# Optimization experiments

Measured on AMD Instinct MI355X. Metric: run time of the kernel, lower is better.

Reference implementation:

```python
import jax, jax.numpy as jnp
import numpy as np

RANK = 10
SLOPE = 0.01  # nn.LeakyReLU default negative_slope


def _leaky(x):
    return jnp.where(x >= 0, x, SLOPE * x)


def _synth(x, aw, ab, weight, bias, ns, w_lat, lid):
    # fmm_modulate_linear with activation='demod'
    c_out, c_in = weight.shape
    styles = aw @ w_lat + ab                      # [(c_in+c_out)*RANK]
    L = styles[: c_out * RANK].reshape(c_out, RANK)
    R = styles[c_out * RANK :].reshape(RANK, c_in)
    mod = (L @ R) * (1.0 / np.sqrt(RANK))          # [c_out, c_in]
    W = weight * (mod + 1.0)
    W = W / (jnp.linalg.norm(W, axis=1, keepdims=True) + 1e-8)
    out = x @ W.T + bias                           # [N, c_out]
    out = _leaky(out)
    noise = jax.random.normal(jax.random.fold_in(jax.random.key(42), lid),
                              out.shape, dtype=out.dtype)
    return out + noise * ns


def setup_inputs() -> dict:
    key = jax.random.key(0)
    N, E, H, IN, OUT, WD = 50000, 800000, 256, 128, 256, 512
    ks = jax.random.split(key, 24)
    s = lambda fan: 1.0 / np.sqrt(fan)
    syn = lambda k0, k1, k2, k3, ci, co: {
        'aw': jax.random.normal(k0, ((ci + co) * RANK, WD)) * s(WD),
        'ab': jnp.zeros(((ci + co) * RANK,)),
        'weight': jax.random.normal(k1, (co, ci)) * s(ci),
        'bias': jax.random.uniform(k2, (co,), minval=-s(ci), maxval=s(ci)),
    }
    le = syn(ks[0], ks[1], ks[2], ks[3], H, H)
    f1 = syn(ks[4], ks[5], ks[6], ks[7], H, H)
    f2 = syn(ks[8], ks[9], ks[10], ks[11], H, OUT)
    return {
        'x': jax.random.normal(ks[12], (N, IN)),
        'edge_index': jax.random.randint(ks[13], (2, E), 0, N, dtype=jnp.int32),
        'w': jax.random.normal(ks[14], (WD,)),
        'node_weight': jax.random.normal(ks[15], (N, H)) * s(N),
        'edge_bias': jax.random.uniform(ks[16], (H,), minval=-s(N), maxval=s(N)),
        'le_aw': le['aw'], 'le_ab': le['ab'], 'le_weight': le['weight'], 'le_bias': le['bias'],
        'le_ns': jnp.zeros(()),
        'cat1_w': jax.random.normal(ks[17], (H, H)) * s(H), 'cat1_b': jnp.zeros((H,)),
        'cat2_w': jax.random.normal(ks[18], (H, H)) * s(H), 'cat2_b': jnp.zeros((H,)),
        'nm_w': jax.random.normal(ks[19], (H, IN)) * s(IN), 'nm_b': jnp.zeros((H,)),
        'f1_aw': f1['aw'], 'f1_ab': f1['ab'], 'f1_weight': f1['weight'], 'f1_bias': f1['bias'],
        'f1_ns': jnp.zeros(()),
        'f2_aw': f2['aw'], 'f2_ab': f2['ab'], 'f2_weight': f2['weight'], 'f2_bias': f2['bias'],
        'f2_ns': jnp.zeros(()),
    }


def reference(x, edge_index, w, node_weight, edge_bias,
              le_aw, le_ab, le_weight, le_bias, le_ns,
              cat1_w, cat1_b, cat2_w, cat2_b, nm_w, nm_b,
              f1_aw, f1_ab, f1_weight, f1_bias, f1_ns,
              f2_aw, f2_ab, f2_weight, f2_bias, f2_ns):
    N = node_weight.shape[0]
    src, dst = edge_index[0], edge_index[1]
    # SparseLinear: scatter-add source node embeddings at destinations
    agg = jax.ops.segment_sum(node_weight[src], dst, num_segments=N) + edge_bias
    out = _synth(agg, le_aw, le_ab, le_weight, le_bias, le_ns, w, 0)
    out = out + (out @ cat1_w.T + cat1_b)
    xn = x @ nm_w.T + nm_b                        # node_mlp (single linear)
    out = out + xn + (xn @ cat2_w.T + cat2_b)
    out = _leaky(out)
    out = _synth(out, f1_aw, f1_ab, f1_weight, f1_bias, f1_ns, w, 1)
    out = _synth(out, f2_aw, f2_ab, f2_weight, f2_bias, f2_ns, w, 2)
    return out
```

## Files before the change

kernel.cpp:

```cpp
#include <hip/hip_runtime.h>
#include <stdint.h>

#define HCH 256
#define INCH 128
#define WDIM 512
#define NRANK 10
#define SLOPE 0.01f

typedef __attribute__((ext_vector_type(16))) float f32x16;
typedef __attribute__((ext_vector_type(8))) short s16x8;

__device__ __forceinline__ float leaky(float v) { return v >= 0.f ? v : SLOPE * v; }

__device__ __forceinline__ void splitf(float v, ushort& h, ushort& l) {
  uint32_t u = __float_as_uint(v);
  uint32_t r = u + 0x7FFFu + ((u >> 16) & 1u);
  h = (ushort)(r >> 16);
  float hf = __uint_as_float((uint32_t)h << 16);
  float d = v - hf;
  uint32_t u2 = __float_as_uint(d);
  uint32_t r2 = u2 + 0x7FFFu + ((u2 >> 16) & 1u);
  l = (ushort)(r2 >> 16);
}

__device__ __forceinline__ int wsi(int o, int k) {
  return (k >> 5) * 8192 + ((k >> 4) & 1) * 4096 + ((k >> 3) & 1) * 2048 + o * 8 + (k & 7);
}

__global__ void k_styles(const float* __restrict__ aw0, const float* __restrict__ ab0,
                         const float* __restrict__ aw1, const float* __restrict__ ab1,
                         const float* __restrict__ aw2, const float* __restrict__ ab2,
                         const float* __restrict__ w, float* __restrict__ styles) {
  int wid = blockIdx.x * 4 + (threadIdx.x >> 6);
  int lane = threadIdx.x & 63;
  int s = wid / 5120;
  int r = wid - s * 5120;
  const float* aw = (s == 0) ? aw0 : (s == 1) ? aw1 : aw2;
  const float* ab = (s == 0) ? ab0 : (s == 1) ? ab1 : ab2;
  const float4* ap = (const float4*)(aw + (size_t)r * WDIM + lane * 8);
  const float4* wp = (const float4*)(w + lane * 8);
  float4 a0 = ap[0], a1 = ap[1], w0 = wp[0], w1 = wp[1];
  float sum = a0.x * w0.x + a0.y * w0.y + a0.z * w0.z + a0.w * w0.w +
              a1.x * w1.x + a1.y * w1.y + a1.z * w1.z + a1.w * w1.w;
#pragma unroll
  for (int off = 32; off > 0; off >>= 1) sum += __shfl_down(sum, off);
  if (lane == 0) styles[wid] = sum + ab[r];
}

__global__ void k_weights(const float* __restrict__ styles,
                          const float* __restrict__ wt0, const float* __restrict__ bs0,
                          const float* __restrict__ wt1, const float* __restrict__ bs1,
                          const float* __restrict__ wt2, const float* __restrict__ bs2,
                          ushort* __restrict__ Wh0, ushort* __restrict__ Wl0,
                          ushort* __restrict__ Wh1, ushort* __restrict__ Wl1,
                          ushort* __restrict__ Wh2, ushort* __restrict__ Wl2,
                          float* __restrict__ biasf) {
  int s = blockIdx.x >> 8;
  int o = blockIdx.x & 255;
  int k = threadIdx.x;
  const float* st = styles + s * 5120;
  const float* wt = (s == 0) ? wt0 : (s == 1) ? wt1 : wt2;
  const float* bs = (s == 0) ? bs0 : (s == 1) ? bs1 : bs2;
  ushort* Wh = (s == 0) ? Wh0 : (s == 1) ? Wh1 : Wh2;
  ushort* Wl = (s == 0) ? Wl0 : (s == 1) ? Wl1 : Wl2;
  float mod = 0.f;
#pragma unroll
  for (int r = 0; r < NRANK; r++)
    mod += st[o * NRANK + r] * st[HCH * NRANK + r * HCH + k];
  mod *= 0.31622776601683794f;
  float wv = wt[o * HCH + k] * (mod + 1.0f);
  __shared__ float red[HCH];
  red[k] = wv * wv;
  __syncthreads();
  for (int t = 128; t > 0; t >>= 1) {
    if (k < t) red[k] += red[k + t];
    __syncthreads();
  }
  float inv = 1.0f / (sqrtf(red[0]) + 1e-8f);
  ushort h, l;
  splitf(wv * inv, h, l);
  int idx = wsi(o, k);
  Wh[idx] = h;
  Wl[idx] = l;
  if (k == 0) biasf[s * HCH + o] = bs[o];
}

__global__ void k_prep(const float* __restrict__ cat1_w, const float* __restrict__ cat1_b,
                       const float* __restrict__ cat2_w, const float* __restrict__ cat2_b,
                       const float* __restrict__ nm_w, const float* __restrict__ nm_b,
                       ushort* __restrict__ M1h, ushort* __restrict__ M1l,
                       ushort* __restrict__ K2h, ushort* __restrict__ K2l,
                       float* __restrict__ b23) {
  int o = blockIdx.x;
  int t = threadIdx.x;
  for (int k = t; k < HCH; k += 128) {
    float m1v = cat1_w[o * HCH + k] + ((k == o) ? 1.f : 0.f);
    ushort h, l;
    splitf(m1v, h, l);
    int idx = wsi(o, k);
    M1h[idx] = h;
    M1l[idx] = l;
  }
  float acc = 0.f;
  for (int k = 0; k < HCH; k++) {
    float m2 = cat2_w[o * HCH + k] + ((k == o) ? 1.f : 0.f);
    acc += m2 * nm_w[k * INCH + t];
  }
  ushort h, l;
  splitf(acc, h, l);
  int idx = wsi(o, t);
  K2h[idx] = h;
  K2l[idx] = l;
  if (t == 0) {
    float bb = cat1_b[o] + cat2_b[o];
    for (int k = 0; k < HCH; k++)
      bb += (cat2_w[o * HCH + k] + ((k == o) ? 1.f : 0.f)) * nm_b[k];
    b23[o] = bb;
  }
}

__global__ void k_zero(int* __restrict__ p, int n) {
  int i = blockIdx.x * blockDim.x + threadIdx.x;
  if (i < n) p[i] = 0;
}
__global__ void k_hist(const int* __restrict__ ei, int* __restrict__ cnt, int E) {
  int e = blockIdx.x * blockDim.x + threadIdx.x;
  if (e < E) atomicAdd(&cnt[ei[E + e]], 1);
}
__global__ void k_bsum(const int* __restrict__ cnt, int* __restrict__ bsum, int N) {
  __shared__ int red[256];
  int t = threadIdx.x;
  int i = blockIdx.x * 256 + t;
  red[t] = (i < N) ? cnt[i] : 0;
  __syncthreads();
  for (int d = 128; d > 0; d >>= 1) {
    if (t < d) red[t] += red[t + d];
    __syncthreads();
  }
  if (t == 0) bsum[blockIdx.x] = red[0];
}
__global__ void k_scanb(int* __restrict__ bsum, int* __restrict__ offsets, int NB,
                        int N, int E) {
  __shared__ int s[256];
  int t = threadIdx.x;
  int v = (t < NB) ? bsum[t] : 0;
  s[t] = v;
  __syncthreads();
  for (int d = 1; d < 256; d <<= 1) {
    int tv = (t >= d) ? s[t - d] : 0;
    __syncthreads();
    s[t] += tv;
    __syncthreads();
  }
  if (t < NB) bsum[t] = s[t] - v;
  if (t == 0) offsets[N] = E;
}
__global__ void k_scanseg(int* __restrict__ cnt, const int* __restrict__ bsum,
                          int* __restrict__ offsets, int N) {
  __shared__ int s[256];
  int t = threadIdx.x;
  int i = blockIdx.x * 256 + t;
  int v = (i < N) ? cnt[i] : 0;
  s[t] = v;
  __syncthreads();
  for (int d = 1; d < 256; d <<= 1) {
    int tv = (t >= d) ? s[t - d] : 0;
    __syncthreads();
    s[t] += tv;
    __syncthreads();
  }
  if (i < N) {
    offsets[i] = bsum[blockIdx.x] + s[t] - v;
    cnt[i] = 0;
  }
}
__global__ void k_place(const int* __restrict__ ei, const int* __restrict__ offsets,
                        int* __restrict__ cur, int* __restrict__ csr, int E) {
  int e = blockIdx.x * blockDim.x + threadIdx.x;
  if (e >= E) return;
  int dst = ei[E + e];
  int pos = atomicAdd(&cur[dst], 1);
  csr[offsets[dst] + pos] = ei[e];
}

__global__ void k_pull(const int* __restrict__ csr, const int* __restrict__ offsets,
                       const float* __restrict__ nw, const float* __restrict__ eb,
                       float* __restrict__ agg, int Mc) {
  int wid = blockIdx.x * 4 + (threadIdx.x >> 6);
  if (wid >= Mc) return;
  int lane = threadIdx.x & 63;
  int s0 = offsets[wid], s1 = offsets[wid + 1];
  float4 a0 = *(const float4*)(eb + lane * 4);
  float4 a1 = make_float4(0.f, 0.f, 0.f, 0.f);
  float4 a2 = make_float4(0.f, 0.f, 0.f, 0.f);
  float4 a3 = make_float4(0.f, 0.f, 0.f, 0.f);
  int j = s0;
  for (; j + 3 < s1; j += 4) {
    int sa = csr[j], sb = csr[j + 1], sc = csr[j + 2], sd = csr[j + 3];
    float4 va = *(const float4*)(nw + (size_t)sa * HCH + lane * 4);
    float4 vb = *(const float4*)(nw + (size_t)sb * HCH + lane * 4);
    float4 vc = *(const float4*)(nw + (size_t)sc * HCH + lane * 4);
    float4 vd = *(const float4*)(nw + (size_t)sd * HCH + lane * 4);
    a0.x += va.x; a0.y += va.y; a0.z += va.z; a0.w += va.w;
    a1.x += vb.x; a1.y += vb.y; a1.z += vb.z; a1.w += vb.w;
    a2.x += vc.x; a2.y += vc.y; a2.z += vc.z; a2.w += vc.w;
    a3.x += vd.x; a3.y += vd.y; a3.z += vd.z; a3.w += vd.w;
  }
  for (; j < s1; j++) {
    int sa = csr[j];
    float4 va = *(const float4*)(nw + (size_t)sa * HCH + lane * 4);
    a0.x += va.x; a0.y += va.y; a0.z += va.z; a0.w += va.w;
  }
  a0.x += a1.x + a2.x + a3.x;
  a0.y += a1.y + a2.y + a3.y;
  a0.z += a1.z + a2.z + a3.z;
  a0.w += a1.w + a2.w + a3.w;
  *(float4*)(agg + (size_t)wid * HCH + lane * 4) = a0;
}


#define CHUNK(PH, PL, c)                                                        \
  {                                                                             \
    const char* _bh = (const char*)(PH) + (c) * 16384 + wlane;                  \
    const char* _bl = (const char*)(PL) + (c) * 16384 + wlane;                  \
    s16x8 bh0 = *(const s16x8*)(_bh);                                           \
    s16x8 bl0 = *(const s16x8*)(_bl);                                           \
    s16x8 bh1 = *(const s16x8*)(_bh + 8192);                                    \
    s16x8 bl1 = *(const s16x8*)(_bl + 8192);                                    \
    int _s0 = (((c) * 4 + kh) ^ cl) << 4;                                       \
    int _s1 = (((c) * 4 + 2 + kh) ^ cl) << 4;                                   \
    s16x8 a0h = *(const s16x8*)(actH + aoff0 + _s0);                            \
    s16x8 a0l = *(const s16x8*)(actL + aoff0 + _s0);                            \
    s16x8 a1h = *(const s16x8*)(actH + aoff1 + _s0);                            \
    s16x8 a1l = *(const s16x8*)(actL + aoff1 + _s0);                            \
    acc0 = __builtin_amdgcn_mfma_f32_32x32x16_bf16(a0h, bh0, acc0, 0, 0, 0);    \
    acc0 = __builtin_amdgcn_mfma_f32_32x32x16_bf16(a0h, bl0, acc0, 0, 0, 0);    \
    acc0 = __builtin_amdgcn_mfma_f32_32x32x16_bf16(a0l, bh0, acc0, 0, 0, 0);    \
    acc1 = __builtin_amdgcn_mfma_f32_32x32x16_bf16(a1h, bh0, acc1, 0, 0, 0);    \
    acc1 = __builtin_amdgcn_mfma_f32_32x32x16_bf16(a1h, bl0, acc1, 0, 0, 0);    \
    acc1 = __builtin_amdgcn_mfma_f32_32x32x16_bf16(a1l, bh0, acc1, 0, 0, 0);    \
    s16x8 c0h = *(const s16x8*)(actH + aoff0 + _s1);                            \
    s16x8 c0l = *(const s16x8*)(actL + aoff0 + _s1);                            \
    s16x8 c1h = *(const s16x8*)(actH + aoff1 + _s1);                            \
    s16x8 c1l = *(const s16x8*)(actL + aoff1 + _s1);                            \
    acc0 = __builtin_amdgcn_mfma_f32_32x32x16_bf16(c0h, bh1, acc0, 0, 0, 0);    \
    acc0 = __builtin_amdgcn_mfma_f32_32x32x16_bf16(c0h, bl1, acc0, 0, 0, 0);    \
    acc0 = __builtin_amdgcn_mfma_f32_32x32x16_bf16(c0l, bh1, acc0, 0, 0, 0);    \
    acc1 = __builtin_amdgcn_mfma_f32_32x32x16_bf16(c1h, bh1, acc1, 0, 0, 0);    \
    acc1 = __builtin_amdgcn_mfma_f32_32x32x16_bf16(c1h, bl1, acc1, 0, 0, 0);    \
    acc1 = __builtin_amdgcn_mfma_f32_32x32x16_bf16(c1l, bh1, acc1, 0, 0, 0);    \
  }

#define EPI_ACT(BIAS)                                                           \
  {                                                                             \
    int _col = w * 32 + cl;                                                     \
    float _bb = (BIAS)[_col];                                                   \
    int _cb = _col & ~1;                                                        \
    _Pragma("unroll") for (int r = 0; r < 16; r++) {                            \
      int _rowf = (r & 3) + 8 * (r >> 2) + 4 * kh;                              \
      _Pragma("unroll") for (int part = 0; part < 2; part++) {                  \
        int _row = part * 32 + _rowf;                                           \
        float _v = (part ? acc1[r] : acc0[r]) + _bb;                            \
        _v = _v >= 0.f ? _v : SLOPE * _v;                                       \
        ushort _h, _l;                                                          \
        splitf(_v, _h, _l);                                                     \
        uint32_t _hl = ((uint32_t)_h << 16) | (uint32_t)_l;                     \
        uint32_t _pr = __shfl_xor(_hl, 1);                                      \
        int _off = _row * 512 + (((_cb >> 3) ^ (_row & 31)) << 4) + (_cb & 7) * 2; \
        uint32_t _wd = (cl & 1) ? ((_pr & 0xFFFFu) | (_hl << 16))               \
                                : ((_hl >> 16) | (_pr & 0xFFFF0000u));          \
        char* _pl = (cl & 1) ? actL : actH;                                     \
        *(uint32_t*)(_pl + _off) = _wd;                                         \
      }                                                                         \
      acc0[r] = 0.f;                                                            \
      acc1[r] = 0.f;                                                            \
    }                                                                           \
  }

__global__ __launch_bounds__(512, 4) void k_fused(
    const float* __restrict__ agg, const float* __restrict__ x,
    const ushort* __restrict__ Wleh, const ushort* __restrict__ Wlel,
    const ushort* __restrict__ M1h, const ushort* __restrict__ M1l,
    const ushort* __restrict__ K2h, const ushort* __restrict__ K2l,
    const ushort* __restrict__ Wf1h, const ushort* __restrict__ Wf1l,
    const ushort* __restrict__ Wf2h, const ushort* __restrict__ Wf2l,
    const float* __restrict__ biasf, const float* __restrict__ b23,
    float* __restrict__ out, int Nn) {
  __shared__ __align__(16) char smem[65536];
  char* actH = smem;
  char* actL = smem + 32768;

  int tid = threadIdx.x;
  int lane = tid & 63;
  int w = tid >> 6;
  int cl = lane & 31;
  int kh = lane >> 5;
  int r0 = blockIdx.x * 64;

  const int wlane = kh * 4096 + (w * 32 + cl) * 16;
  const int aoff0 = cl * 512;
  const int aoff1 = (32 + cl) * 512;

  {
    int gr = tid >> 3;
    int gn = r0 + gr;
    if (gn >= Nn) gn = Nn - 1;
    int cb = 4 * (tid & 7);
    const float* ap = agg + (size_t)gn * HCH + cb;
#pragma unroll
    for (int q = 0; q < 8; q++) {
      float4 v = *(const float4*)(ap + 32 * q);
      int col = cb + 32 * q;
      ushort h0, l0, h1, l1, h2, l2, h3, l3;
      splitf(v.x, h0, l0); splitf(v.y, h1, l1);
      splitf(v.z, h2, l2); splitf(v.w, h3, l3);
      uint2 hh = make_uint2((uint32_t)h0 | ((uint32_t)h1 << 16),
                            (uint32_t)h2 | ((uint32_t)h3 << 16));
      uint2 ll = make_uint2((uint32_t)l0 | ((uint32_t)l1 << 16),
                            (uint32_t)l2 | ((uint32_t)l3 << 16));
      int off = gr * 512 + (((col >> 3) ^ (gr & 31)) << 4) + (col & 7) * 2;
      *(uint2*)(actH + off) = hh;
      *(uint2*)(actL + off) = ll;
    }
  }
  __syncthreads();

  f32x16 acc0, acc1;
#pragma unroll
  for (int i = 0; i < 16; i++) { acc0[i] = 0.f; acc1[i] = 0.f; }

#pragma unroll
  for (int c = 0; c < 8; c++) CHUNK(Wleh, Wlel, c);
  __syncthreads();
  EPI_ACT(biasf);
  __syncthreads();

#pragma unroll
  for (int c = 0; c < 8; c++) CHUNK(M1h, M1l, c);
  __syncthreads();
  {
    int gr = tid >> 3;
    int gn = r0 + gr;
    if (gn >= Nn) gn = Nn - 1;
    int cb = 4 * (tid & 7);
    const float* xp = x + (size_t)gn * INCH + cb;
#pragma unroll
    for (int q = 0; q < 4; q++) {
      float4 v = *(const float4*)(xp + 32 * q);
      int col = cb + 32 * q;
      ushort h0, l0, h1, l1, h2, l2, h3, l3;
      splitf(v.x, h0, l0); splitf(v.y, h1, l1);
      splitf(v.z, h2, l2); splitf(v.w, h3, l3);
      uint2 hh = make_uint2((uint32_t)h0 | ((uint32_t)h1 << 16),
                            (uint32_t)h2 | ((uint32_t)h3 << 16));
      uint2 ll = make_uint2((uint32_t)l0 | ((uint32_t)l1 << 16),
                            (uint32_t)l2 | ((uint32_t)l3 << 16));
      int off = gr * 512 + (((col >> 3) ^ (gr & 31)) << 4) + (col & 7) * 2;
      *(uint2*)(actH + off) = hh;
      *(uint2*)(actL + off) = ll;
    }
  }
  __syncthreads();

#pragma unroll
  for (int c = 0; c < 4; c++) CHUNK(K2h, K2l, c);
  __syncthreads();
  EPI_ACT(b23);
  __syncthreads();

#pragma unroll
  for (int c = 0; c < 8; c++) CHUNK(Wf1h, Wf1l, c);
  __syncthreads();
  EPI_ACT(biasf + HCH);
  __syncthreads();

#pragma unroll
  for (int c = 0; c < 8; c++) CHUNK(Wf2h, Wf2l, c);
  {
    const float* _bs = biasf + 2 * HCH;
    int col = w * 32 + cl;
    float bb = _bs[col];
#pragma unroll
    for (int r = 0; r < 16; r++) {
      int rowf = (r & 3) + 8 * (r >> 2) + 4 * kh;
      int g0 = r0 + rowf;
      int g1 = r0 + 32 + rowf;
      if (g0 < Nn) {
        float v = acc0[r] + bb;
        out[(size_t)g0 * HCH + col] = v >= 0.f ? v : SLOPE * v;
      }
      if (g1 < Nn) {
        float v = acc1[r] + bb;
        out[(size_t)g1 * HCH + col] = v >= 0.f ? v : SLOPE * v;
      }
    }
  }
}

extern "C" void kernel_launch(void* const* d_in, const int* in_sizes, int n_in,
                              void* d_out, int out_size, void* d_ws, size_t ws_size,
                              hipStream_t stream) {
  const float* x      = (const float*)d_in[0];
  const int*   ei     = (const int*)d_in[1];
  const float* w      = (const float*)d_in[2];
  const float* nw     = (const float*)d_in[3];
  const float* eb     = (const float*)d_in[4];
  const float* le_aw  = (const float*)d_in[5];
  const float* le_ab  = (const float*)d_in[6];
  const float* le_w   = (const float*)d_in[7];
  const float* le_b   = (const float*)d_in[8];
  const float* cat1_w = (const float*)d_in[10];
  const float* cat1_b = (const float*)d_in[11];
  const float* cat2_w = (const float*)d_in[12];
  const float* cat2_b = (const float*)d_in[13];
  const float* nm_w   = (const float*)d_in[14];
  const float* nm_b   = (const float*)d_in[15];
  const float* f1_aw  = (const float*)d_in[16];
  const float* f1_ab  = (const float*)d_in[17];
  const float* f1_w   = (const float*)d_in[18];
  const float* f1_b   = (const float*)d_in[19];
  const float* f2_aw  = (const float*)d_in[21];
  const float* f2_ab  = (const float*)d_in[22];
  const float* f2_w   = (const float*)d_in[23];
  const float* f2_b   = (const float*)d_in[24];

  const int N = in_sizes[3] / HCH;
  const int E = in_sizes[1] / 2;
  const int NB = (N + 255) / 256;

  uint8_t* ws = (uint8_t*)d_ws;
  float*  styles = (float*)(ws + 1024);
  float*  biasf  = (float*)(ws + 65536);
  float*  b23    = (float*)(ws + 69632);
  ushort* Wleh   = (ushort*)(ws + 131072);
  ushort* Wlel   = (ushort*)(ws + 262144);
  ushort* Wf1h   = (ushort*)(ws + 393216);
  ushort* Wf1l   = (ushort*)(ws + 524288);
  ushort* Wf2h   = (ushort*)(ws + 655360);
  ushort* Wf2l   = (ushort*)(ws + 786432);
  ushort* M1h    = (ushort*)(ws + 917504);
  ushort* M1l    = (ushort*)(ws + 1048576);
  ushort* K2h    = (ushort*)(ws + 1179648);
  ushort* K2l    = (ushort*)(ws + 1245184);
  int*    cnt    = (int*)(ws + 1376256);
  int*    bsum   = (int*)(ws + 1376256 + 262144);
  int*    offsets= (int*)(ws + 1376256 + 262144 + 4096);
  int*    csr    = (int*)(ws + 1376256 + 262144 + 4096 + 262144);
  size_t aggoff  = 1376256 + 262144 + 4096 + 262144 + (size_t)E * 4 + 65536;
  aggoff = (aggoff + 1023) & ~(size_t)1023;
  float*  agg    = (float*)(ws + aggoff);

  k_styles<<<3840, 256, 0, stream>>>(le_aw, le_ab, f1_aw, f1_ab, f2_aw, f2_ab, w, styles);
  k_weights<<<768, 256, 0, stream>>>(styles, le_w, le_b, f1_w, f1_b, f2_w, f2_b,
                                     Wleh, Wlel, Wf1h, Wf1l, Wf2h, Wf2l, biasf);
  k_prep<<<256, 128, 0, stream>>>(cat1_w, cat1_b, cat2_w, cat2_b, nm_w, nm_b,
                                  M1h, M1l, K2h, K2l, b23);

  int eb256 = (E + 255) / 256;
  k_zero<<<NB, 256, 0, stream>>>(cnt, N);
  k_hist<<<eb256, 256, 0, stream>>>(ei, cnt, E);
  k_bsum<<<NB, 256, 0, stream>>>(cnt, bsum, N);
  k_scanb<<<1, 256, 0, stream>>>(bsum, offsets, NB, N, E);
  k_scanseg<<<NB, 256, 0, stream>>>(cnt, bsum, offsets, N);
  k_place<<<eb256, 256, 0, stream>>>(ei, offsets, cnt, csr, E);

  k_pull<<<(N + 3) / 4, 256, 0, stream>>>(csr, offsets, nw, eb, agg, N);
  k_fused<<<(N + 63) / 64, 512, 0, stream>>>(agg, x,
                                             Wleh, Wlel, M1h, M1l, K2h, K2l,
                                             Wf1h, Wf1l, Wf2h, Wf2l,
                                             biasf, b23, (float*)d_out, N);
}
```

Baseline: 522.8 us.

## Merge setup kernels into persistent megakernel with grid barriers; prefetch weights in fused GEMM

Replaces the nine small preprocessing launches (styles, weight demodulation, cat/node-MLP prep, CSR histogram, scan and placement) with one persistent 256-block kernel whose phases are separated by a software grid barrier on an atomic counter. The aim is to remove per-launch overhead and idle gaps between the tiny kernels. Separately, the fused MFMA kernel now double-buffers the B-weight register loads one chunk ahead, including across stage boundaries, and raises wave priority around the MFMA groups to hide global load latency. Risks: the grid barrier deadlocks if all 256 blocks of 1024 threads cannot be co-resident. The extra prefetch registers may also lower occupancy of the fused kernel.

```diff
diff --git a/kernel.cpp b/kernel.cpp
--- a/kernel.cpp
+++ b/kernel.cpp
@@ -27,160 +27,213 @@
   return (k >> 5) * 8192 + ((k >> 4) & 1) * 4096 + ((k >> 3) & 1) * 2048 + o * 8 + (k & 7);
 }
 
-__global__ void k_styles(const float* __restrict__ aw0, const float* __restrict__ ab0,
-                         const float* __restrict__ aw1, const float* __restrict__ ab1,
-                         const float* __restrict__ aw2, const float* __restrict__ ab2,
-                         const float* __restrict__ w, float* __restrict__ styles) {
-  int wid = blockIdx.x * 4 + (threadIdx.x >> 6);
-  int lane = threadIdx.x & 63;
-  int s = wid / 5120;
-  int r = wid - s * 5120;
-  const float* aw = (s == 0) ? aw0 : (s == 1) ? aw1 : aw2;
-  const float* ab = (s == 0) ? ab0 : (s == 1) ? ab1 : ab2;
-  const float4* ap = (const float4*)(aw + (size_t)r * WDIM + lane * 8);
-  const float4* wp = (const float4*)(w + lane * 8);
-  float4 a0 = ap[0], a1 = ap[1], w0 = wp[0], w1 = wp[1];
-  float sum = a0.x * w0.x + a0.y * w0.y + a0.z * w0.z + a0.w * w0.w +
-              a1.x * w1.x + a1.y * w1.y + a1.z * w1.z + a1.w * w1.w;
-#pragma unroll
-  for (int off = 32; off > 0; off >>= 1) sum += __shfl_down(sum, off);
-  if (lane == 0) styles[wid] = sum + ab[r];
-}
-
-__global__ void k_weights(const float* __restrict__ styles,
-                          const float* __restrict__ wt0, const float* __restrict__ bs0,
-                          const float* __restrict__ wt1, const float* __restrict__ bs1,
-                          const float* __restrict__ wt2, const float* __restrict__ bs2,
-                          ushort* __restrict__ Wh0, ushort* __restrict__ Wl0,
-                          ushort* __restrict__ Wh1, ushort* __restrict__ Wl1,
-                          ushort* __restrict__ Wh2, ushort* __restrict__ Wl2,
-                          float* __restrict__ biasf) {
-  int s = blockIdx.x >> 8;
-  int o = blockIdx.x & 255;
-  int k = threadIdx.x;
-  const float* st = styles + s * 5120;
-  const float* wt = (s == 0) ? wt0 : (s == 1) ? wt1 : wt2;
-  const float* bs = (s == 0) ? bs0 : (s == 1) ? bs1 : bs2;
-  ushort* Wh = (s == 0) ? Wh0 : (s == 1) ? Wh1 : Wh2;
-  ushort* Wl = (s == 0) ? Wl0 : (s == 1) ? Wl1 : Wl2;
-  float mod = 0.f;
-#pragma unroll
-  for (int r = 0; r < NRANK; r++)
-    mod += st[o * NRANK + r] * st[HCH * NRANK + r * HCH + k];
-  mod *= 0.31622776601683794f;
-  float wv = wt[o * HCH + k] * (mod + 1.0f);
-  __shared__ float red[HCH];
-  red[k] = wv * wv;
-  __syncthreads();
-  for (int t = 128; t > 0; t >>= 1) {
-    if (k < t) red[k] += red[k + t];
-    __syncthreads();
-  }
-  float inv = 1.0f / (sqrtf(red[0]) + 1e-8f);
-  ushort h, l;
-  splitf(wv * inv, h, l);
-  int idx = wsi(o, k);
-  Wh[idx] = h;
-  Wl[idx] = l;
-  if (k == 0) biasf[s * HCH + o] = bs[o];
-}
-
-__global__ void k_prep(const float* __restrict__ cat1_w, const float* __restrict__ cat1_b,
-                       const float* __restrict__ cat2_w, const float* __restrict__ cat2_b,
-                       const float* __restrict__ nm_w, const float* __restrict__ nm_b,
-                       ushort* __restrict__ M1h, ushort* __restrict__ M1l,
-                       ushort* __restrict__ K2h, ushort* __restrict__ K2l,
-                       float* __restrict__ b23) {
-  int o = blockIdx.x;
-  int t = threadIdx.x;
-  for (int k = t; k < HCH; k += 128) {
-    float m1v = cat1_w[o * HCH + k] + ((k == o) ? 1.f : 0.f);
-    ushort h, l;
-    splitf(m1v, h, l);
-    int idx = wsi(o, k);
-    M1h[idx] = h;
-    M1l[idx] = l;
-  }
-  float acc = 0.f;
-  for (int k = 0; k < HCH; k++) {
-    float m2 = cat2_w[o * HCH + k] + ((k == o) ? 1.f : 0.f);
-    acc += m2 * nm_w[k * INCH + t];
-  }
-  ushort h, l;
-  splitf(acc, h, l);
-  int idx = wsi(o, t);
-  K2h[idx] = h;
-  K2l[idx] = l;
-  if (t == 0) {
-    float bb = cat1_b[o] + cat2_b[o];
-    for (int k = 0; k < HCH; k++)
+__device__ __forceinline__ void gbar(int* bar, int nblk) {
+  __syncthreads();
+  if (threadIdx.x == 0) {
+    int g = __hip_atomic_load(bar + 1, __ATOMIC_RELAXED, __HIP_MEMORY_SCOPE_AGENT);
+    __threadfence();
+    int a = __hip_atomic_fetch_add(bar, 1, __ATOMIC_ACQ_REL, __HIP_MEMORY_SCOPE_AGENT);
+    if (a == nblk - 1) {
+      __hip_atomic_store(bar, 0, __ATOMIC_RELAXED, __HIP_MEMORY_SCOPE_AGENT);
+      __hip_atomic_fetch_add(bar + 1, 1, __ATOMIC_RELEASE, __HIP_MEMORY_SCOPE_AGENT);
+    } else {
+      while (__hip_atomic_load(bar + 1, __ATOMIC_ACQUIRE, __HIP_MEMORY_SCOPE_AGENT) == g)
+        __builtin_amdgcn_s_sleep(8);
+    }
+  }
+  __syncthreads();
+  __threadfence();
+}
+
+__global__ __launch_bounds__(1024, 4) void k_mega(
+    const float* __restrict__ aw0, const float* __restrict__ ab0,
+    const float* __restrict__ aw1, const float* __restrict__ ab1,
+    const float* __restrict__ aw2, const float* __restrict__ ab2,
+    const float* __restrict__ wvec, float* __restrict__ styles,
+    const float* __restrict__ wt0, const float* __restrict__ bs0,
+    const float* __restrict__ wt1, const float* __restrict__ bs1,
+    const float* __restrict__ wt2, const float* __restrict__ bs2,
+    ushort* __restrict__ Wh0, ushort* __restrict__ Wl0,
+    ushort* __restrict__ Wh1, ushort* __restrict__ Wl1,
+    ushort* __restrict__ Wh2, ushort* __restrict__ Wl2,
+    float* __restrict__ biasf,
+    const float* __restrict__ cat1_w, const float* __restrict__ cat1_b,
+    const float* __restrict__ cat2_w, const float* __restrict__ cat2_b,
+    const float* __restrict__ nm_w, const float* __restrict__ nm_b,
+    ushort* __restrict__ M1h, ushort* __restrict__ M1l,
+    ushort* __restrict__ K2h, ushort* __restrict__ K2l,
+    float* __restrict__ b23,
+    const int* __restrict__ ei, int* __restrict__ cnt, int* __restrict__ bsum,
+    int* __restrict__ offsets, int* __restrict__ csr,
+    int* bar, int N, int E) {
+  int tid = threadIdx.x;
+  int lane = tid & 63;
+  int gw = blockIdx.x * 16 + (tid >> 6);
+  int gt = blockIdx.x * 1024 + tid;
+
+  for (int r = gw; r < 15360; r += 4096) {
+    int s = r / 5120;
+    int rr = r - s * 5120;
+    const float* aw = (s == 0) ? aw0 : (s == 1) ? aw1 : aw2;
+    const float* ab = (s == 0) ? ab0 : (s == 1) ? ab1 : ab2;
+    const float4* ap = (const float4*)(aw + (size_t)rr * WDIM + lane * 8);
+    const float4* wp = (const float4*)(wvec + lane * 8);
+    float4 a0 = ap[0], a1 = ap[1], w0 = wp[0], w1 = wp[1];
+    float sum = a0.x * w0.x + a0.y * w0.y + a0.z * w0.z + a0.w * w0.w +
+                a1.x * w1.x + a1.y * w1.y + a1.z * w1.z + a1.w * w1.w;
+#pragma unroll
+    for (int off = 32; off > 0; off >>= 1) sum += __shfl_down(sum, off);
+    if (lane == 0) styles[r] = sum + ab[rr];
+  }
+  if (gt < N) cnt[gt] = 0;
+  if (gt == 0) offsets[N] = E;
+  gbar(bar, 256);
+
+  if (gw < 768) {
+    int s = gw >> 8, o = gw & 255;
+    const float* st = styles + s * 5120;
+    const float* wt = (s == 0) ? wt0 : (s == 1) ? wt1 : wt2;
+    const float* bs = (s == 0) ? bs0 : (s == 1) ? bs1 : bs2;
+    ushort* Wh = (s == 0) ? Wh0 : (s == 1) ? Wh1 : Wh2;
+    ushort* Wl = (s == 0) ? Wl0 : (s == 1) ? Wl1 : Wl2;
+    int k0 = lane * 4;
+    float modv[4] = {0.f, 0.f, 0.f, 0.f};
+#pragma unroll
+    for (int r = 0; r < NRANK; r++) {
+      float a = st[o * NRANK + r];
+#pragma unroll
+      for (int j = 0; j < 4; j++) modv[j] += a * st[HCH * NRANK + r * HCH + k0 + j];
+    }
+    float wv[4];
+    float ssq = 0.f;
+#pragma unroll
+    for (int j = 0; j < 4; j++) {
+      wv[j] = wt[o * HCH + k0 + j] * (modv[j] * 0.31622776601683794f + 1.0f);
+      ssq += wv[j] * wv[j];
+    }
+#pragma unroll
+    for (int off = 32; off > 0; off >>= 1) ssq += __shfl_down(ssq, off);
+    ssq = __shfl(ssq, 0);
+    float inv = 1.0f / (sqrtf(ssq) + 1e-8f);
+#pragma unroll
+    for (int j = 0; j < 4; j++) {
+      ushort h, l;
+      splitf(wv[j] * inv, h, l);
+      int idx = wsi(o, k0 + j);
+      Wh[idx] = h;
+      Wl[idx] = l;
+    }
+    if (lane == 0) biasf[s * HCH + o] = bs[o];
+  } else if (gw < 1024) {
+    int o = gw - 768;
+    int k0 = lane * 4;
+#pragma unroll
+    for (int j = 0; j < 4; j++) {
+      int k = k0 + j;
+      float m1v = cat1_w[o * HCH + k] + ((k == o) ? 1.f : 0.f);
+      ushort h, l;
+      splitf(m1v, h, l);
+      int idx = wsi(o, k);
+      M1h[idx] = h;
+      M1l[idx] = l;
+    }
+    for (int tt = lane; tt < INCH; tt += 64) {
+      float acc = 0.f;
+      for (int k = 0; k < HCH; k++) {
+        float m2 = cat2_w[o * HCH + k] + ((k == o) ? 1.f : 0.f);
+        acc += m2 * nm_w[k * INCH + tt];
+      }
+      ushort h, l;
+      splitf(acc, h, l);
+      int idx = wsi(o, tt);
+      K2h[idx] = h;
+      K2l[idx] = l;
+    }
+    float bb = 0.f;
+    for (int k = lane; k < HCH; k += 64)
       bb += (cat2_w[o * HCH + k] + ((k == o) ? 1.f : 0.f)) * nm_b[k];
-    b23[o] = bb;
-  }
-}
-
-__global__ void k_zero(int* __restrict__ p, int n) {
-  int i = blockIdx.x * blockDim.x + threadIdx.x;
-  if (i < n) p[i] = 0;
-}
-__global__ void k_hist(const int* __restrict__ ei, int* __restrict__ cnt, int E) {
-  int e = blockIdx.x * blockDim.x + threadIdx.x;
-  if (e < E) atomicAdd(&cnt[ei[E + e]], 1);
-}
-__global__ void k_bsum(const int* __restrict__ cnt, int* __restrict__ bsum, int N) {
-  __shared__ int red[256];
-  int t = threadIdx.x;
-  int i = blockIdx.x * 256 + t;
-  red[t] = (i < N) ? cnt[i] : 0;
-  __syncthreads();
-  for (int d = 128; d > 0; d >>= 1) {
-    if (t < d) red[t] += red[t + d];
-    __syncthreads();
-  }
-  if (t == 0) bsum[blockIdx.x] = red[0];
-}
-__global__ void k_scanb(int* __restrict__ bsum, int* __restrict__ offsets, int NB,
-                        int N, int E) {
-  __shared__ int s[256];
-  int t = threadIdx.x;
-  int v = (t < NB) ? bsum[t] : 0;
-  s[t] = v;
-  __syncthreads();
-  for (int d = 1; d < 256; d <<= 1) {
-    int tv = (t >= d) ? s[t - d] : 0;
-    __syncthreads();
-    s[t] += tv;
-    __syncthreads();
-  }
-  if (t < NB) bsum[t] = s[t] - v;
-  if (t == 0) offsets[N] = E;
-}
-__global__ void k_scanseg(int* __restrict__ cnt, const int* __restrict__ bsum,
-                          int* __restrict__ offsets, int N) {
-  __shared__ int s[256];
-  int t = threadIdx.x;
-  int i = blockIdx.x * 256 + t;
-  int v = (i < N) ? cnt[i] : 0;
-  s[t] = v;
-  __syncthreads();
-  for (int d = 1; d < 256; d <<= 1) {
-    int tv = (t >= d) ? s[t - d] : 0;
-    __syncthreads();
-    s[t] += tv;
-    __syncthreads();
-  }
-  if (i < N) {
-    offsets[i] = bsum[blockIdx.x] + s[t] - v;
-    cnt[i] = 0;
-  }
-}
-__global__ void k_place(const int* __restrict__ ei, const int* __restrict__ offsets,
-                        int* __restrict__ cur, int* __restrict__ csr, int E) {
-  int e = blockIdx.x * blockDim.x + threadIdx.x;
-  if (e >= E) return;
-  int dst = ei[E + e];
-  int pos = atomicAdd(&cur[dst], 1);
-  csr[offsets[dst] + pos] = ei[e];
+#pragma unroll
+    for (int off = 32; off > 0; off >>= 1) bb += __shfl_down(bb, off);
+    if (lane == 0) b23[o] = cat1_b[o] + cat2_b[o] + bb;
+  } else {
+    int base = (gw - 1024) * 64 + lane;
+    for (int e = base; e < E; e += 3072 * 64) atomicAdd(&cnt[ei[E + e]], 1);
+  }
+  gbar(bar, 256);
+
+  int NCH = (N + 255) >> 8;
+  if (gw < NCH) {
+    int v = 0;
+#pragma unroll
+    for (int j = 0; j < 4; j++) {
+      int i = gw * 256 + lane + j * 64;
+      v += (i < N) ? cnt[i] : 0;
+    }
+#pragma unroll
+    for (int off = 32; off > 0; off >>= 1) v += __shfl_down(v, off);
+    if (lane == 0) bsum[gw] = v;
+  }
+  gbar(bar, 256);
+
+  if (gw == 0) {
+    int v[4];
+    int lsum = 0;
+#pragma unroll
+    for (int j = 0; j < 4; j++) {
+      int i = lane * 4 + j;
+      v[j] = (i < NCH) ? bsum[i] : 0;
+      lsum += v[j];
+    }
+    int inc = lsum;
+#pragma unroll
+    for (int d = 1; d < 64; d <<= 1) {
+      int t = __shfl_up(inc, d);
+      if (lane >= d) inc += t;
+    }
+    int run = inc - lsum;
+#pragma unroll
+    for (int j = 0; j < 4; j++) {
+      int i = lane * 4 + j;
+      int nv = v[j];
+      if (i < NCH) bsum[i] = run;
+      run += nv;
+    }
+  }
+  gbar(bar, 256);
+
+  if (gw < NCH) {
+    int v[4];
+    int lsum = 0;
+#pragma unroll
+    for (int j = 0; j < 4; j++) {
+      int i = gw * 256 + lane * 4 + j;
+      v[j] = (i < N) ? cnt[i] : 0;
+      lsum += v[j];
+    }
+    int inc = lsum;
+#pragma unroll
+    for (int d = 1; d < 64; d <<= 1) {
+      int t = __shfl_up(inc, d);
+      if (lane >= d) inc += t;
+    }
+    int run = bsum[gw] + inc - lsum;
+#pragma unroll
+    for (int j = 0; j < 4; j++) {
+      int i = gw * 256 + lane * 4 + j;
+      if (i < N) {
+        offsets[i] = run;
+        cnt[i] = 0;
+      }
+      run += v[j];
+    }
+  }
+  gbar(bar, 256);
+
+  for (int e = gt; e < E; e += 262144) {
+    int dst = ei[E + e];
+    int pos = atomicAdd(&cnt[dst], 1);
+    csr[offsets[dst] + pos] = ei[e];
+  }
 }
 
 __global__ void k_pull(const int* __restrict__ csr, const int* __restrict__ offsets,
@@ -219,36 +272,55 @@
 }
 
 
-#define CHUNK(PH, PL, c)                                                        \
+#define BLOADS(SH0, SL0, SH1, SL1, PH, PL, C)                                  \
+  {                                                                            \
+    const char* _bh = (const char*)(PH) + (C) * 16384 + wlane;                 \
+    const char* _bl = (const char*)(PL) + (C) * 16384 + wlane;                 \
+    SH0 = *(const s16x8*)(_bh);                                                \
+    SL0 = *(const s16x8*)(_bl);                                                \
+    SH1 = *(const s16x8*)(_bh + 8192);                                         \
+    SL1 = *(const s16x8*)(_bl + 8192);                                         \
+  }
+
+#define CMFMA(BH0, BL0, BH1, BL1, C)                                            \
   {                                                                             \
-    const char* _bh = (const char*)(PH) + (c) * 16384 + wlane;                  \
-    const char* _bl = (const char*)(PL) + (c) * 16384 + wlane;                  \
-    s16x8 bh0 = *(const s16x8*)(_bh);                                           \
-    s16x8 bl0 = *(const s16x8*)(_bl);                                           \
-    s16x8 bh1 = *(const s16x8*)(_bh + 8192);                                    \
-    s16x8 bl1 = *(const s16x8*)(_bl + 8192);                                    \
-    int _s0 = (((c) * 4 + kh) ^ cl) << 4;                                       \
-    int _s1 = (((c) * 4 + 2 + kh) ^ cl) << 4;                                   \
+    int _s0 = ((((C) * 4 + kh) ^ cl) << 4);                                     \
+    int _s1 = ((((C) * 4 + 2 + kh) ^ cl) << 4);                                 \
     s16x8 a0h = *(const s16x8*)(actH + aoff0 + _s0);                            \
     s16x8 a0l = *(const s16x8*)(actL + aoff0 + _s0);                            \
     s16x8 a1h = *(const s16x8*)(actH + aoff1 + _s0);                            \
     s16x8 a1l = *(const s16x8*)(actL + aoff1 + _s0);                            \
-    acc0 = __builtin_amdgcn_mfma_f32_32x32x16_bf16(a0h, bh0, acc0, 0, 0, 0);    \
-    acc0 = __builtin_amdgcn_mfma_f32_32x32x16_bf16(a0h, bl0, acc0, 0, 0, 0);    \
-    acc0 = __builtin_amdgcn_mfma_f32_32x32x16_bf16(a0l, bh0, acc0, 0, 0, 0);    \
-    acc1 = __builtin_amdgcn_mfma_f32_32x32x16_bf16(a1h, bh0, acc1, 0, 0, 0);    \
-    acc1 = __builtin_amdgcn_mfma_f32_32x32x16_bf16(a1h, bl0, acc1, 0, 0, 0);    \
-    acc1 = __builtin_amdgcn_mfma_f32_32x32x16_bf16(a1l, bh0, acc1, 0, 0, 0);    \
+    acc0 = __builtin_amdgcn_mfma_f32_32x32x16_bf16(a0h, BH0, acc0, 0, 0, 0);    \
+    acc0 = __builtin_amdgcn_mfma_f32_32x32x16_bf16(a0h, BL0, acc0, 0, 0, 0);    \
+    acc0 = __builtin_amdgcn_mfma_f32_32x32x16_bf16(a0l, BH0, acc0, 0, 0, 0);    \
+    acc1 = __builtin_amdgcn_mfma_f32_32x32x16_bf16(a1h, BH0, acc1, 0, 0, 0);    \
+    acc1 = __builtin_amdgcn_mfma_f32_32x32x16_bf16(a1h, BL0, acc1, 0, 0, 0);    \
+    acc1 = __builtin_amdgcn_mfma_f32_32x32x16_bf16(a1l, BH0, acc1, 0, 0, 0);    \
     s16x8 c0h = *(const s16x8*)(actH + aoff0 + _s1);                            \
     s16x8 c0l = *(const s16x8*)(actL + aoff0 + _s1);                            \
     s16x8 c1h = *(const s16x8*)(actH + aoff1 + _s1);                            \
     s16x8 c1l = *(const s16x8*)(actL + aoff1 + _s1);                            \
-    acc0 = __builtin_amdgcn_mfma_f32_32x32x16_bf16(c0h, bh1, acc0, 0, 0, 0);    \
-    acc0 = __builtin_amdgcn_mfma_f32_32x32x16_bf16(c0h, bl1, acc0, 0, 0, 0);    \
-    acc0 = __builtin_amdgcn_mfma_f32_32x32x16_bf16(c0l, bh1, acc0, 0, 0, 0);    \
-    acc1 = __builtin_amdgcn_mfma_f32_32x32x16_bf16(c1h, bh1, acc1, 0, 0, 0);    \
-    acc1 = __builtin_amdgcn_mfma_f32_32x32x16_bf16(c1h, bl1, acc1, 0, 0, 0);    \
-    acc1 = __builtin_amdgcn_mfma_f32_32x32x16_bf16(c1l, bh1, acc1, 0, 0, 0);    \
+    acc0 = __builtin_amdgcn_mfma_f32_32x32x16_bf16(c0h, BH1, acc0, 0, 0, 0);    \
+    acc0 = __builtin_amdgcn_mfma_f32_32x32x16_bf16(c0h, BL1, acc0, 0, 0, 0);    \
+    acc0 = __builtin_amdgcn_mfma_f32_32x32x16_bf16(c0l, BH1, acc0, 0, 0, 0);    \
+    acc1 = __builtin_amdgcn_mfma_f32_32x32x16_bf16(c1h, BH1, acc1, 0, 0, 0);    \
+    acc1 = __builtin_amdgcn_mfma_f32_32x32x16_bf16(c1h, BL1, acc1, 0, 0, 0);    \
+    acc1 = __builtin_amdgcn_mfma_f32_32x32x16_bf16(c1l, BH1, acc1, 0, 0, 0);    \
+  }
+
+#define STAGE(NC, PH, PL, NPH, NPL)                                             \
+  _Pragma("unroll")                                                             \
+  for (int c = 0; c < (NC); c += 2) {                                           \
+    __builtin_amdgcn_s_setprio(1);                                              \
+    CMFMA(pbh0, pbl0, pbh1, pbl1, c);                                           \
+    __builtin_amdgcn_s_setprio(0);                                              \
+    if (c + 2 < (NC)) { BLOADS(pbh0, pbl0, pbh1, pbl1, PH, PL, c + 2); }        \
+    else if ((NPH) != nullptr) { BLOADS(pbh0, pbl0, pbh1, pbl1, NPH, NPL, c + 2 - (NC)); } \
+    __builtin_amdgcn_s_setprio(1);                                              \
+    CMFMA(qbh0, qbl0, qbh1, qbl1, c + 1);                                       \
+    __builtin_amdgcn_s_setprio(0);                                              \
+    if (c + 3 < (NC)) { BLOADS(qbh0, qbl0, qbh1, qbl1, PH, PL, c + 3); }        \
+    else if ((NPH) != nullptr) { BLOADS(qbh0, qbl0, qbh1, qbl1, NPH, NPL, c + 3 - (NC)); } \
   }
 
 #define EPI_ACT(BIAS)                                                           \
@@ -301,6 +373,12 @@
   const int aoff0 = cl * 512;
   const int aoff1 = (32 + cl) * 512;
 
+  s16x8 pbh0, pbl0, pbh1, pbl1;
+  s16x8 qbh0, qbl0, qbh1, qbl1;
+
+  BLOADS(pbh0, pbl0, pbh1, pbl1, Wleh, Wlel, 0);
+  BLOADS(qbh0, qbl0, qbh1, qbl1, Wleh, Wlel, 1);
+
   {
     int gr = tid >> 3;
     int gn = r0 + gr;
@@ -329,14 +407,12 @@
 #pragma unroll
   for (int i = 0; i < 16; i++) { acc0[i] = 0.f; acc1[i] = 0.f; }
 
-#pragma unroll
-  for (int c = 0; c < 8; c++) CHUNK(Wleh, Wlel, c);
+  STAGE(8, Wleh, Wlel, M1h, M1l)
   __syncthreads();
   EPI_ACT(biasf);
   __syncthreads();
 
-#pragma unroll
-  for (int c = 0; c < 8; c++) CHUNK(M1h, M1l, c);
+  STAGE(8, M1h, M1l, K2h, K2l)
   __syncthreads();
   {
     int gr = tid >> 3;
@@ -362,20 +438,17 @@
   }
   __syncthreads();
 
-#pragma unroll
-  for (int c = 0; c < 4; c++) CHUNK(K2h, K2l, c);
+  STAGE(4, K2h, K2l, Wf1h, Wf1l)
   __syncthreads();
   EPI_ACT(b23);
   __syncthreads();
 
-#pragma unroll
-  for (int c = 0; c < 8; c++) CHUNK(Wf1h, Wf1l, c);
+  STAGE(8, Wf1h, Wf1l, Wf2h, Wf2l)
   __syncthreads();
   EPI_ACT(biasf + HCH);
   __syncthreads();
 
-#pragma unroll
-  for (int c = 0; c < 8; c++) CHUNK(Wf2h, Wf2l, c);
+  STAGE(8, Wf2h, Wf2l, (const ushort*)nullptr, (const ushort*)nullptr)
   {
     const float* _bs = biasf + 2 * HCH;
     int col = w * 32 + cl;
@@ -426,9 +499,9 @@
 
   const int N = in_sizes[3] / HCH;
   const int E = in_sizes[1] / 2;
-  const int NB = (N + 255) / 256;
 
   uint8_t* ws = (uint8_t*)d_ws;
+  int*    bar    = (int*)ws;
   float*  styles = (float*)(ws + 1024);
   float*  biasf  = (float*)(ws + 65536);
   float*  b23    = (float*)(ws + 69632);
@@ -450,20 +523,13 @@
   aggoff = (aggoff + 1023) & ~(size_t)1023;
   float*  agg    = (float*)(ws + aggoff);
 
-  k_styles<<<3840, 256, 0, stream>>>(le_aw, le_ab, f1_aw, f1_ab, f2_aw, f2_ab, w, styles);
-  k_weights<<<768, 256, 0, stream>>>(styles, le_w, le_b, f1_w, f1_b, f2_w, f2_b,
-                                     Wleh, Wlel, Wf1h, Wf1l, Wf2h, Wf2l, biasf);
-  k_prep<<<256, 128, 0, stream>>>(cat1_w, cat1_b, cat2_w, cat2_b, nm_w, nm_b,
-                                  M1h, M1l, K2h, K2l, b23);
-
-  int eb256 = (E + 255) / 256;
-  k_zero<<<NB, 256, 0, stream>>>(cnt, N);
-  k_hist<<<eb256, 256, 0, stream>>>(ei, cnt, E);
-  k_bsum<<<NB, 256, 0, stream>>>(cnt, bsum, N);
-  k_scanb<<<1, 256, 0, stream>>>(bsum, offsets, NB, N, E);
-  k_scanseg<<<NB, 256, 0, stream>>>(cnt, bsum, offsets, N);
-  k_place<<<eb256, 256, 0, stream>>>(ei, offsets, cnt, csr, E);
-
+  hipMemsetAsync(bar, 0, 64, stream);
+  k_mega<<<256, 1024, 0, stream>>>(le_aw, le_ab, f1_aw, f1_ab, f2_aw, f2_ab, w,
+                                   styles, le_w, le_b, f1_w, f1_b, f2_w, f2_b,
+                                   Wleh, Wlel, Wf1h, Wf1l, Wf2h, Wf2l, biasf,
+                                   cat1_w, cat1_b, cat2_w, cat2_b, nm_w, nm_b,
+                                   M1h, M1l, K2h, K2l, b23,
+                                   ei, cnt, bsum, offsets, csr, bar, N, E);
   k_pull<<<(N + 3) / 4, 256, 0, stream>>>(csr, offsets, nw, eb, agg, N);
   k_fused<<<(N + 63) / 64, 512, 0, stream>>>(agg, x,
                                              Wleh, Wlel, M1h, M1l, K2h, K2l,
```

New measurement: 987.9 us. +89.0%, slower.
